# Optimization experiments

Measured on AMD Instinct MI355X. Metric: run time of the kernel, lower is better.

## Reference

```python
import jax, jax.numpy as jnp
import numpy as np
from jax import lax

DIM = 384
HEADS = 8
HEAD_DIM = DIM // HEADS
EPS = 1e-06


def setup_inputs() -> dict:
    key = jax.random.key(0)
    ks = jax.random.split(key, 16)
    B, N, C = 8, 4096, DIM
    s = 0.02
    inp = {
        "x": jax.random.normal(ks[0], (B, N, C), jnp.float32),
        "wq": jax.random.normal(ks[1], (C, C), jnp.float32) * s,
        "bq": jnp.zeros((C,), jnp.float32),
        "wk": jax.random.normal(ks[2], (C, C), jnp.float32) * s,
        "bk": jnp.zeros((C,), jnp.float32),
        "wv": jax.random.normal(ks[3], (C, C), jnp.float32) * s,
        "bv": jnp.zeros((C,), jnp.float32),
        "wg": jax.random.normal(ks[4], (C, C), jnp.float32) * s,
        "bg": jnp.zeros((C,), jnp.float32),
        "wo": jax.random.normal(ks[5], (C, C), jnp.float32) * s,
        "bo": jnp.zeros((C,), jnp.float32),
        "temperature": jnp.ones((HEADS, 1, 1), jnp.float32),
        "dw_w": jax.random.normal(ks[6], (C, 1, 3, 3), jnp.float32) * s,  # depthwise 3x3
        "dw_b": jnp.zeros((C,), jnp.float32),
        "pw_w": jax.random.normal(ks[7], (C, C), jnp.float32) * s,        # pointwise 1x1
        "pw_b": jnp.zeros((C,), jnp.float32),
    }
    return inp


def _phi(x):
    # exp(x - max) over last dim, numerically stable
    return jnp.exp(x - jnp.max(x, axis=-1, keepdims=True))


def _token_mixer(x, dw_w, dw_b, pw_w, pw_b):
    B, N, C = x.shape
    H = W = int(np.sqrt(N))
    feat = x.transpose(0, 2, 1).reshape(B, C, H, W)
    feat = lax.conv_general_dilated(
        feat, dw_w, window_strides=(1, 1), padding=((1, 1), (1, 1)),
        feature_group_count=C, dimension_numbers=("NCHW", "OIHW", "NCHW"))
    feat = feat + dw_b[None, :, None, None]
    feat = jnp.einsum("bchw,oc->bohw", feat, pw_w) + pw_b[None, :, None, None]
    return feat.reshape(B, C, N).transpose(0, 2, 1)


def reference(x, wq, bq, wk, bk, wv, bv, wg, bg, wo, bo, temperature,
              dw_w, dw_b, pw_w, pw_b):
    B, N, C = x.shape
    residual = x
    x = x + _token_mixer(x, dw_w, dw_b, pw_w, pw_b)

    def heads(y):  # [B,N,C] -> [B,H,N,d]
        return y.reshape(B, N, HEADS, HEAD_DIM).transpose(0, 2, 1, 3)

    q = heads(jnp.einsum("bnc,oc->bno", x, wq) + bq)
    k = heads(jnp.einsum("bnc,oc->bno", x, wk) + bk)
    v = heads(jnp.einsum("bnc,oc->bno", x, wv) + bv)
    g = heads(jnp.einsum("bnc,oc->bno", x, wg) + bg)

    q = _phi(q * temperature[None])       # temperature: [H,1,1] broadcasts over [B,H,N,d]
    k = _phi(k)
    v = v * jax.nn.sigmoid(g)

    kv = jnp.einsum("bhnd,bhne->bhde", k, v)     # [B,H,d,d]
    k_sum = jnp.sum(k, axis=2)                   # [B,H,d]
    num = jnp.einsum("bhnd,bhde->bhne", q, kv)   # [B,H,N,d]
    den = jnp.einsum("bhnd,bhd->bhn", q, k_sum)[..., None] + EPS
    out = num / den

    out = out.transpose(0, 2, 1, 3).reshape(B, N, C)
    out = jnp.einsum("bnc,oc->bno", out, wo) + bo
    return out + 0.0 * residual
```

## Files before the change

### kernel.cpp

```cpp
#include <hip/hip_runtime.h>
#include <math.h>

#define EPSF 1e-6f

typedef __attribute__((ext_vector_type(8))) short bf16x8;
typedef __attribute__((ext_vector_type(4))) float f32x4;
typedef unsigned short u16;
typedef unsigned int u32;

#define MFMA16(a,b,c) __builtin_amdgcn_mfma_f32_16x16x32_bf16((a),(b),(c),0,0,0)

__device__ __forceinline__ u16 f2bf(float f){
  u32 x = __builtin_bit_cast(u32, f);
  u32 r = (x + 0x7fffu + ((x >> 16) & 1u)) >> 16;
  return (u16)r;
}
__device__ __forceinline__ void gll16(const void* g, void* l){
  __builtin_amdgcn_global_load_lds(
      (const __attribute__((address_space(1))) u32*)g,
      (__attribute__((address_space(3))) u32*)l, 16, 0, 0);
}

__global__ __launch_bounds__(256) void k0_prep(
    const float* __restrict__ wq, const float* __restrict__ bq,
    const float* __restrict__ wk, const float* __restrict__ bk,
    const float* __restrict__ wv, const float* __restrict__ bv,
    const float* __restrict__ wg, const float* __restrict__ bg,
    const float* __restrict__ pw_w, const float* __restrict__ wo,
    u16* __restrict__ wpack, u16* __restrict__ pwb, u16* __restrict__ wob,
    float* __restrict__ bpack, float* __restrict__ kvacc, float* __restrict__ ksumacc)
{
  int idx = blockIdx.x*256 + threadIdx.x;
  const int NW = 1536*384;
  if (idx < NW) {
    int r = idx / 384, c = idx - r*384;
    int h = r / 192, s = (r % 192)/48, d = r % 48;
    const float* w = (s==0)?wq:(s==1)?wk:(s==2)?wv:wg;
    wpack[idx] = f2bf(w[(h*48+d)*384 + c]);
    if (c==0){
      const float* b = (s==0)?bq:(s==1)?bk:(s==2)?bv:bg;
      bpack[r] = b[h*48+d];
    }
  } else if (idx < NW + 147456) {
    pwb[idx - NW] = f2bf(pw_w[idx - NW]);
  } else if (idx < NW + 2*147456) {
    wob[idx - NW - 147456] = f2bf(wo[idx - NW - 147456]);
  } else if (idx < NW + 2*147456 + 147456) {
    kvacc[idx - NW - 2*147456] = 0.f;
  } else if (idx < NW + 2*147456 + 147456 + 3072) {
    ksumacc[idx - NW - 2*147456 - 147456] = 0.f;
  }
}

__global__ __launch_bounds__(256) void k1_dw(
    const float* __restrict__ x, const float* __restrict__ dw_w,
    const float* __restrict__ dw_b, u16* __restrict__ t)
{
  int idx = blockIdx.x*256 + threadIdx.x;
  int c4 = idx % 96; int rest = idx / 96;
  int jg = rest & 15; rest >>= 4;
  int i = rest & 63; int b = rest >> 6;
  int c0 = c4*4, j0 = jg*4;
  float wf[36];
  {
    const float4* wp = (const float4*)(dw_w + c0*9);
    #pragma unroll
    for (int k=0;k<9;k++){
      float4 v = wp[k];
      wf[4*k] = v.x; wf[4*k+1] = v.y; wf[4*k+2] = v.z; wf[4*k+3] = v.w;
    }
  }
  float4 bias = *(const float4*)(dw_b + c0);
  float acc[4][4];
  #pragma unroll
  for (int tk=0;tk<4;tk++){
    acc[tk][0]=bias.x; acc[tk][1]=bias.y; acc[tk][2]=bias.z; acc[tk][3]=bias.w;
  }
  const float* xb = x + ((size_t)b<<12)*384;
  #pragma unroll
  for (int di=-1; di<=1; ++di){
    int ii = i+di; if ((unsigned)ii >= 64u) continue;
    #pragma unroll
    for (int dj=-1; dj<=4; ++dj){
      int jj = j0+dj; if ((unsigned)jj >= 64u) continue;
      float4 xv = *(const float4*)(xb + (size_t)((ii<<6)+jj)*384 + c0);
      #pragma unroll
      for (int tk=0;tk<4;tk++){
        const int dd = dj - tk;
        if (dd < -1 || dd > 1) continue;
        const int tap = (di+1)*3 + (dd+1);
        acc[tk][0] = fmaf(xv.x, wf[0*9+tap], acc[tk][0]);
        acc[tk][1] = fmaf(xv.y, wf[1*9+tap], acc[tk][1]);
        acc[tk][2] = fmaf(xv.z, wf[2*9+tap], acc[tk][2]);
        acc[tk][3] = fmaf(xv.w, wf[3*9+tap], acc[tk][3]);
      }
    }
  }
  int mbase = (b<<12) + (i<<6) + j0;
  #pragma unroll
  for (int tk=0;tk<4;tk++){
    ushort4 o; o.x=f2bf(acc[tk][0]); o.y=f2bf(acc[tk][1]);
    o.z=f2bf(acc[tk][2]); o.w=f2bf(acc[tk][3]);
    *(ushort4*)(t + (size_t)(mbase+tk)*384 + c0) = o;
  }
}

__global__ __launch_bounds__(256) void k2_gemm_pw(
    const u16* __restrict__ t, const u16* __restrict__ pwb,
    const float* __restrict__ x, const float* __restrict__ pw_b,
    u16* __restrict__ xm)
{
  __shared__ __align__(16) u16 As[128*64];
  __shared__ __align__(16) u16 Bs[128*64];
  const int m0 = blockIdx.x * 128;
  const int n0 = blockIdx.y * 128;
  const int tid = threadIdx.x, w = tid>>6, l = tid&63;
  const int lc = l & 15, hi = l >> 4;
  const int osw = ((l&7) ^ (l>>3))*16;
  const f32x4 zf = {0.f,0.f,0.f,0.f};
  f32x4 acc[4][4];
  #pragma unroll
  for (int i=0;i<4;i++)
    #pragma unroll
    for (int j=0;j<4;j++) acc[i][j] = zf;

  for (int k0=0; k0<384; k0+=64) {
    #pragma unroll
    for (int i=0;i<4;i++){
      int ch = w*4+i;
      int row = ch*8 + (l>>3);
      gll16((const char*)t   + ((size_t)(m0+row)*384 + k0)*2 + osw, (char*)As + ch*1024);
      gll16((const char*)pwb + ((size_t)(n0+row)*384 + k0)*2 + osw, (char*)Bs + ch*1024);
    }
    __syncthreads();
    const int wr = (w>>1)*64, wc = (w&1)*64;
    #pragma unroll
    for (int kk=0; kk<64; kk+=32){
      const int sc = (((kk>>3)+hi) ^ (lc&7))*8;
      bf16x8 a[4], bb[4];
      #pragma unroll
      for (int i=0;i<4;i++) a[i]  = *(const bf16x8*)&As[(wr + i*16 + lc)*64 + sc];
      #pragma unroll
      for (int j=0;j<4;j++) bb[j] = *(const bf16x8*)&Bs[(wc + j*16 + lc)*64 + sc];
      #pragma unroll
      for (int i=0;i<4;i++)
        #pragma unroll
        for (int j=0;j<4;j++)
          acc[i][j] = MFMA16(a[i], bb[j], acc[i][j]);
    }
    __syncthreads();
  }
  const int wr=(w>>1)*64, wc=(w&1)*64;
  #pragma unroll
  for (int j=0;j<4;j++){
    int n = n0 + wc + j*16 + lc;
    float bias = pw_b[n];
    #pragma unroll
    for (int i=0;i<4;i++)
      #pragma unroll
      for (int r=0;r<4;r++){
        int m = m0 + wr + i*16 + hi*4 + r;
        float v = acc[i][j][r] + x[(size_t)m*384 + n] + bias;
        xm[(size_t)m*384 + n] = f2bf(v);
      }
  }
}

__global__ __launch_bounds__(256) void k3_gemm_qkvg(
    const u16* __restrict__ xm, const u16* __restrict__ wpack,
    const float* __restrict__ bpack, const float* __restrict__ temperature,
    u16* __restrict__ qh, float* __restrict__ kvacc, float* __restrict__ ksumacc)
{
  __shared__ __align__(16) u16 smem[40960];
  const int m0 = blockIdx.x * 128;
  const int h  = blockIdx.y;
  const int tid = threadIdx.x, w = tid>>6, l = tid&63;
  const int lc = l & 15, hi = l >> 4;
  const int osw = ((l&7) ^ (l>>3))*16;
  const f32x4 zf = {0.f,0.f,0.f,0.f};
  f32x4 acc[2][12];
  #pragma unroll
  for (int i=0;i<2;i++)
    #pragma unroll
    for (int j=0;j<12;j++) acc[i][j] = zf;

  const int arow = (w*4)*8 + (l>>3);
  const int brow = (w*6)*8 + (l>>3);

  #define K3_STAGE(T, BUF) do {                                                \
    const int k0_ = (T)*64;                                                    \
    char* Ab_ = (char*)(smem + (BUF)*8192);                                    \
    char* Bb_ = (char*)(smem + 16384 + (BUF)*12288);                           \
    _Pragma("unroll")                                                          \
    for (int i=0;i<4;i++)                                                      \
      gll16((const char*)xm + ((size_t)(m0+arow+i*8)*384 + k0_)*2 + osw,       \
            Ab_ + (w*4+i)*1024);                                               \
    _Pragma("unroll")                                                          \
    for (int i=0;i<6;i++)                                                      \
      gll16((const char*)wpack + ((size_t)(h*192+brow+i*8)*384 + k0_)*2 + osw, \
            Bb_ + (w*6+i)*1024);                                               \
  } while(0)

  K3_STAGE(0, 0);
  __syncthreads();
  int cur = 0;
  const int rbase = w*32;
  for (int t=0; t<6; ++t){
    if (t < 5) K3_STAGE(t+1, cur^1);
    const u16* Ab = smem + cur*8192;
    const u16* Bb = smem + 16384 + cur*12288;
    #pragma unroll
    for (int kk=0; kk<64; kk+=32){
      const int sc = (((kk>>3)+hi) ^ (lc&7))*8;
      bf16x8 a0 = *(const bf16x8*)&Ab[(rbase +      lc)*64 + sc];
      bf16x8 a1 = *(const bf16x8*)&Ab[(rbase + 16 + lc)*64 + sc];
      #pragma unroll
      for (int j=0;j<12;j++){
        bf16x8 bb = *(const bf16x8*)&Bb[(j*16 + lc)*64 + sc];
        acc[0][j] = MFMA16(a0, bb, acc[0][j]);
        acc[1][j] = MFMA16(a1, bb, acc[1][j]);
      }
    }
    __syncthreads();
    cur ^= 1;
  }
  #undef K3_STAGE

  const float tq = temperature[h];
  const int b = m0 >> 12;
  const size_t bh = (size_t)b*8 + h;
  const int bb0 = h*192;
  float biasq[3], biask[3], biasv[3], biasg[3];
  #pragma unroll
  for (int j=0;j<3;j++){
    biasq[j] = bpack[bb0       + j*16 + lc];
    biask[j] = bpack[bb0 + 48  + j*16 + lc];
    biasv[j] = bpack[bb0 + 96  + j*16 + lc];
    biasg[j] = bpack[bb0 + 144 + j*16 + lc];
  }
  u16* kT = smem;
  u16* vT = smem + 6528;
  float ksp[3] = {0.f, 0.f, 0.f};

  #pragma unroll
  for (int i=0;i<2;i++){
    ushort4 kst[3], vst[3];
    #pragma unroll
    for (int r=0;r<4;r++){
      int m = m0 + w*32 + i*16 + hi*4 + r;
      int n = m & 4095;
      size_t rowq = (bh*4096 + n)*64;
      float q0=(acc[i][0][r]+biasq[0])*tq;
      float q1=(acc[i][1][r]+biasq[1])*tq;
      float q2=(acc[i][2][r]+biasq[2])*tq;
      float mx = fmaxf(q0,fmaxf(q1,q2));
      mx = fmaxf(mx, __shfl_xor(mx,1,64));
      mx = fmaxf(mx, __shfl_xor(mx,2,64));
      mx = fmaxf(mx, __shfl_xor(mx,4,64));
      mx = fmaxf(mx, __shfl_xor(mx,8,64));
      qh[rowq +      lc] = f2bf(expf(q0-mx));
      qh[rowq + 16 + lc] = f2bf(expf(q1-mx));
      qh[rowq + 32 + lc] = f2bf(expf(q2-mx));
      qh[rowq + 48 + lc] = 0;
      float s0=acc[i][3][r]+biask[0];
      float s1=acc[i][4][r]+biask[1];
      float s2=acc[i][5][r]+biask[2];
      float mk = fmaxf(s0,fmaxf(s1,s2));
      mk = fmaxf(mk, __shfl_xor(mk,1,64));
      mk = fmaxf(mk, __shfl_xor(mk,2,64));
      mk = fmaxf(mk, __shfl_xor(mk,4,64));
      mk = fmaxf(mk, __shfl_xor(mk,8,64));
      float k0e = expf(s0-mk), k1e = expf(s1-mk), k2e = expf(s2-mk);
      ksp[0] += k0e; ksp[1] += k1e; ksp[2] += k2e;
      u16 kq0=f2bf(k0e), kq1=f2bf(k1e), kq2=f2bf(k2e);
      u16 vq[3];
      #pragma unroll
      for (int j=0;j<3;j++){
        float vv = acc[i][6+j][r] + biasv[j];
        float gg = acc[i][9+j][r] + biasg[j];
        float sg = 1.f/(1.f + expf(-gg));
        vq[j] = f2bf(vv*sg);
      }
      if (r==0){ kst[0].x=kq0; kst[1].x=kq1; kst[2].x=kq2; vst[0].x=vq[0]; vst[1].x=vq[1]; vst[2].x=vq[2]; }
      if (r==1){ kst[0].y=kq0; kst[1].y=kq1; kst[2].y=kq2; vst[0].y=vq[0]; vst[1].y=vq[1]; vst[2].y=vq[2]; }
      if (r==2){ kst[0].z=kq0; kst[1].z=kq1; kst[2].z=kq2; vst[0].z=vq[0]; vst[1].z=vq[1]; vst[2].z=vq[2]; }
      if (r==3){ kst[0].w=kq0; kst[1].w=kq1; kst[2].w=kq2; vst[0].w=vq[0]; vst[1].w=vq[1]; vst[2].w=vq[2]; }
    }
    int mb = w*32 + i*16 + hi*4;
    #pragma unroll
    for (int j=0;j<3;j++){
      *(ushort4*)&kT[(j*16+lc)*136 + mb] = kst[j];
      *(ushort4*)&vT[(j*16+lc)*136 + mb] = vst[j];
    }
  }
  __syncthreads();

  bf16x8 af[3], bfv[3];
  #pragma unroll
  for (int da=0;da<3;da++) af[da]  = *(const bf16x8*)&kT[(da*16+lc)*136 + w*32 + hi*8];
  #pragma unroll
  for (int eb=0;eb<3;eb++) bfv[eb] = *(const bf16x8*)&vT[(eb*16+lc)*136 + w*32 + hi*8];
  f32x4 a2[3][3];
  #pragma unroll
  for (int da=0;da<3;da++)
    #pragma unroll
    for (int eb=0;eb<3;eb++)
      a2[da][eb] = MFMA16(af[da], bfv[eb], zf);
  __syncthreads();
  float* pb = (float*)smem + w*2304;
  #pragma unroll
  for (int da=0;da<3;da++)
    #pragma unroll
    for (int eb=0;eb<3;eb++)
      #pragma unroll
      for (int rr=0;rr<4;rr++)
        pb[(da*16 + hi*4 + rr)*48 + eb*16 + lc] = a2[da][eb][rr];
  __syncthreads();
  float* p0 = (float*)smem;
  for (int u=tid; u<2304; u+=256){
    float s = p0[u] + p0[2304+u] + p0[4608+u] + p0[6912+u];
    atomicAdd(kvacc + bh*2304 + u, s);
  }
  #pragma unroll
  for (int j=0;j<3;j++){
    ksp[j] += __shfl_xor(ksp[j],16,64);
    ksp[j] += __shfl_xor(ksp[j],32,64);
  }
  if (hi==0){
    atomicAdd(ksumacc + bh*48 +      lc, ksp[0]);
    atomicAdd(ksumacc + bh*48 + 16 + lc, ksp[1]);
    atomicAdd(ksumacc + bh*48 + 32 + lc, ksp[2]);
  }
}

__global__ __launch_bounds__(256) void k5_red(
    const float* __restrict__ kvacc, const float* __restrict__ ksumacc,
    u16* __restrict__ kvp)
{
  int bh = blockIdx.x, tid = threadIdx.x;
  for (int u=tid; u<4096; u+=256){
    int e = u >> 6, d = u & 63;
    float v = 0.f;
    if (e < 48 && d < 48)       v = kvacc[(size_t)bh*2304 + d*48 + e];
    else if (e == 48 && d < 48) v = ksumacc[bh*48 + d];
    kvp[((size_t)bh*64 + e)*64 + d] = f2bf(v);
  }
}

__global__ __launch_bounds__(256) void k6_num(
    const u16* __restrict__ qh, const u16* __restrict__ kvp, u16* __restrict__ ah)
{
  __shared__ __align__(16) u16 As[256*64];
  __shared__ __align__(16) u16 Bs[64*64];
  const int bh = blockIdx.x >> 4, nc = blockIdx.x & 15;
  const int tid = threadIdx.x, w = tid>>6, l = tid&63;
  const int lc = l & 15, hi = l >> 4;
  const f32x4 zf = {0.f,0.f,0.f,0.f};
  const u16* gq = qh + ((size_t)bh*4096 + nc*256)*64;
  #pragma unroll
  for (int it=0; it<8; ++it){
    int s = it*256 + tid;
    int row = s>>3, c = s&7, g = c ^ (row&7);
    ((uint4*)As)[s] = *(const uint4*)(gq + (size_t)row*64 + g*8);
  }
  const u16* gk = kvp + (size_t)bh*4096;
  #pragma unroll
  for (int it=0; it<2; ++it){
    int s = it*256 + tid;
    int row = s>>3, c = s&7, g = c ^ (row&7);
    ((uint4*)Bs)[s] = *(const uint4*)(gk + (size_t)row*64 + g*8);
  }
  __syncthreads();
  f32x4 acc[4][4];
  #pragma unroll
  for (int i=0;i<4;i++)
    #pragma unroll
    for (int j=0;j<4;j++) acc[i][j] = zf;
  const int rbase = w*64;
  #pragma unroll
  for (int kk=0; kk<64; kk+=32){
    const int sc = (((kk>>3)+hi) ^ (lc&7))*8;
    bf16x8 a[4], bb[4];
    #pragma unroll
    for (int i=0;i<4;i++) a[i]  = *(const bf16x8*)&As[(rbase + i*16 + lc)*64 + sc];
    #pragma unroll
    for (int j=0;j<4;j++) bb[j] = *(const bf16x8*)&Bs[(j*16 + lc)*64 + sc];
    #pragma unroll
    for (int i=0;i<4;i++)
      #pragma unroll
      for (int j=0;j<4;j++)
        acc[i][j] = MFMA16(a[i], bb[j], acc[i][j]);
  }
  const int b = bh >> 3, h = bh & 7;
  #pragma unroll
  for (int i=0;i<4;i++){
    #pragma unroll
    for (int r=0;r<4;r++){
      float den = __shfl(acc[i][3][r], l & 48, 64) + EPSF;
      float rd = 1.f/den;
      int n = nc*256 + rbase + i*16 + hi*4 + r;
      size_t ob = ((size_t)b*4096 + n)*384 + h*48;
      ah[ob +      lc] = f2bf(acc[i][0][r]*rd);
      ah[ob + 16 + lc] = f2bf(acc[i][1][r]*rd);
      ah[ob + 32 + lc] = f2bf(acc[i][2][r]*rd);
    }
  }
}

__global__ __launch_bounds__(256) void k7_gemm_out(
    const u16* __restrict__ ah, const u16* __restrict__ wob,
    const float* __restrict__ bo, float* __restrict__ out)
{
  __shared__ __align__(16) u16 As[128*64];
  __shared__ __align__(16) u16 Bs[128*64];
  const int m0 = blockIdx.x * 128;
  const int n0 = blockIdx.y * 128;
  const int tid = threadIdx.x, w = tid>>6, l = tid&63;
  const int lc = l & 15, hi = l >> 4;
  const int osw = ((l&7) ^ (l>>3))*16;
  const f32x4 zf = {0.f,0.f,0.f,0.f};
  f32x4 acc[4][4];
  #pragma unroll
  for (int i=0;i<4;i++)
    #pragma unroll
    for (int j=0;j<4;j++) acc[i][j] = zf;

  for (int k0=0; k0<384; k0+=64) {
    #pragma unroll
    for (int i=0;i<4;i++){
      int ch = w*4+i;
      int row = ch*8 + (l>>3);
      gll16((const char*)ah  + ((size_t)(m0+row)*384 + k0)*2 + osw, (char*)As + ch*1024);
      gll16((const char*)wob + ((size_t)(n0+row)*384 + k0)*2 + osw, (char*)Bs + ch*1024);
    }
    __syncthreads();
    const int wr = (w>>1)*64, wc = (w&1)*64;
    #pragma unroll
    for (int kk=0; kk<64; kk+=32){
      const int sc = (((kk>>3)+hi) ^ (lc&7))*8;
      bf16x8 a[4], bb[4];
      #pragma unroll
      for (int i=0;i<4;i++) a[i]  = *(const bf16x8*)&As[(wr + i*16 + lc)*64 + sc];
      #pragma unroll
      for (int j=0;j<4;j++) bb[j] = *(const bf16x8*)&Bs[(wc + j*16 + lc)*64 + sc];
      #pragma unroll
      for (int i=0;i<4;i++)
        #pragma unroll
        for (int j=0;j<4;j++)
          acc[i][j] = MFMA16(a[i], bb[j], acc[i][j]);
    }
    __syncthreads();
  }
  const int wr=(w>>1)*64, wc=(w&1)*64;
  #pragma unroll
  for (int j=0;j<4;j++){
    int n = n0 + wc + j*16 + lc;
    float bias = bo[n];
    #pragma unroll
    for (int i=0;i<4;i++)
      #pragma unroll
      for (int r=0;r<4;r++){
        int m = m0 + wr + i*16 + hi*4 + r;
        out[(size_t)m*384 + n] = acc[i][j][r] + bias;
      }
  }
}

extern "C" void kernel_launch(void* const* d_in, const int* in_sizes, int n_in,
                              void* d_out, int out_size, void* d_ws, size_t ws_size,
                              hipStream_t stream)
{
  const float* x    = (const float*)d_in[0];
  const float* wq   = (const float*)d_in[1];
  const float* bq   = (const float*)d_in[2];
  const float* wk   = (const float*)d_in[3];
  const float* bk   = (const float*)d_in[4];
  const float* wv   = (const float*)d_in[5];
  const float* bv   = (const float*)d_in[6];
  const float* wg   = (const float*)d_in[7];
  const float* bg   = (const float*)d_in[8];
  const float* wo   = (const float*)d_in[9];
  const float* bo   = (const float*)d_in[10];
  const float* temp = (const float*)d_in[11];
  const float* dw_w = (const float*)d_in[12];
  const float* dw_b = (const float*)d_in[13];
  const float* pw_w = (const float*)d_in[14];
  const float* pw_b = (const float*)d_in[15];
  float* out = (float*)d_out;
  char* ws = (char*)d_ws;

  u16*   t       = (u16*)(ws + 0);
  u16*   xm      = (u16*)(ws + 25165824);
  u16*   qh      = (u16*)(ws + 50331648);
  u16*   wpack   = (u16*)(ws + 83886080);
  u16*   pwb     = (u16*)(ws + 85065728);
  u16*   wob     = (u16*)(ws + 85360640);
  float* bpack   = (float*)(ws + 85655552);
  float* kvacc   = (float*)(ws + 85661696);
  float* ksumacc = (float*)(ws + 86251520);
  u16*   kvp     = (u16*)(ws + 86263808);

  k0_prep<<<4044, 256, 0, stream>>>(wq,bq,wk,bk,wv,bv,wg,bg,pw_w,wo,
                                    wpack,pwb,wob,bpack,kvacc,ksumacc);
  k1_dw<<<3072, 256, 0, stream>>>(x, dw_w, dw_b, t);
  k2_gemm_pw<<<dim3(256,3), 256, 0, stream>>>(t, pwb, x, pw_b, xm);
  k3_gemm_qkvg<<<dim3(256,8), 256, 0, stream>>>(xm, wpack, bpack, temp, qh, kvacc, ksumacc);
  k5_red<<<64, 256, 0, stream>>>(kvacc, ksumacc, kvp);
  k6_num<<<1024, 256, 0, stream>>>(qh, kvp, t );
  k7_gemm_out<<<dim3(256,3), 256, 0, stream>>>(t, wob, bo, out);
}
```

Before: 190.9 us.

## Replace kv atomics with per-tile partial sums reduced in k5; drop q max-subtraction

k3 no longer atomically accumulates the kv and k-sum statistics into global buffers. Each block now writes its own partial tile into a scratch area that reuses the dead t region, and k5 sums the 32 partials per batch-head before packing. The zeroing of the accumulators in k0 is removed. This trades millions of contended global atomics for plain stores plus an extra 19MB read pass in k5. The per-row max subtraction for q is also dropped, since it cancels in num/den, which saves shuffles but risks exp overflow for large q.

New measurement: 186.6 us. 1.02x faster.

```diff
diff --git a/kernel.cpp b/kernel.cpp
--- a/kernel.cpp
+++ b/kernel.cpp
@@ -28,7 +28,7 @@
     const float* __restrict__ wg, const float* __restrict__ bg,
     const float* __restrict__ pw_w, const float* __restrict__ wo,
     u16* __restrict__ wpack, u16* __restrict__ pwb, u16* __restrict__ wob,
-    float* __restrict__ bpack, float* __restrict__ kvacc, float* __restrict__ ksumacc)
+    float* __restrict__ bpack)
 {
   int idx = blockIdx.x*256 + threadIdx.x;
   const int NW = 1536*384;
@@ -45,10 +45,6 @@
     pwb[idx - NW] = f2bf(pw_w[idx - NW]);
   } else if (idx < NW + 2*147456) {
     wob[idx - NW - 147456] = f2bf(wo[idx - NW - 147456]);
-  } else if (idx < NW + 2*147456 + 147456) {
-    kvacc[idx - NW - 2*147456] = 0.f;
-  } else if (idx < NW + 2*147456 + 147456 + 3072) {
-    ksumacc[idx - NW - 2*147456 - 147456] = 0.f;
   }
 }
 
@@ -169,7 +165,7 @@
 __global__ __launch_bounds__(256) void k3_gemm_qkvg(
     const u16* __restrict__ xm, const u16* __restrict__ wpack,
     const float* __restrict__ bpack, const float* __restrict__ temperature,
-    u16* __restrict__ qh, float* __restrict__ kvacc, float* __restrict__ ksumacc)
+    u16* __restrict__ qh, float* __restrict__ pkv, float* __restrict__ pks)
 {
   __shared__ __align__(16) u16 smem[40960];
   const int m0 = blockIdx.x * 128;
@@ -228,6 +224,7 @@
 
   const float tq = temperature[h];
   const int b = m0 >> 12;
+  const int mtile = (m0 >> 7) & 31;
   const size_t bh = (size_t)b*8 + h;
   const int bb0 = h*192;
   float biasq[3], biask[3], biasv[3], biasg[3];
@@ -253,14 +250,9 @@
       float q0=(acc[i][0][r]+biasq[0])*tq;
       float q1=(acc[i][1][r]+biasq[1])*tq;
       float q2=(acc[i][2][r]+biasq[2])*tq;
-      float mx = fmaxf(q0,fmaxf(q1,q2));
-      mx = fmaxf(mx, __shfl_xor(mx,1,64));
-      mx = fmaxf(mx, __shfl_xor(mx,2,64));
-      mx = fmaxf(mx, __shfl_xor(mx,4,64));
-      mx = fmaxf(mx, __shfl_xor(mx,8,64));
-      qh[rowq +      lc] = f2bf(expf(q0-mx));
-      qh[rowq + 16 + lc] = f2bf(expf(q1-mx));
-      qh[rowq + 32 + lc] = f2bf(expf(q2-mx));
+      qh[rowq +      lc] = f2bf(expf(q0));
+      qh[rowq + 16 + lc] = f2bf(expf(q1));
+      qh[rowq + 32 + lc] = f2bf(expf(q2));
       qh[rowq + 48 + lc] = 0;
       float s0=acc[i][3][r]+biask[0];
       float s1=acc[i][4][r]+biask[1];
@@ -316,33 +308,60 @@
       for (int rr=0;rr<4;rr++)
         pb[(da*16 + hi*4 + rr)*48 + eb*16 + lc] = a2[da][eb][rr];
   __syncthreads();
-  float* p0 = (float*)smem;
-  for (int u=tid; u<2304; u+=256){
-    float s = p0[u] + p0[2304+u] + p0[4608+u] + p0[6912+u];
-    atomicAdd(kvacc + bh*2304 + u, s);
+  {
+    float* p0 = (float*)smem;
+    float* dst = pkv + ((size_t)bh*32 + mtile)*2304;
+    for (int u=tid; u<2304; u+=256)
+      dst[u] = p0[u] + p0[2304+u] + p0[4608+u] + p0[6912+u];
   }
   #pragma unroll
   for (int j=0;j<3;j++){
     ksp[j] += __shfl_xor(ksp[j],16,64);
     ksp[j] += __shfl_xor(ksp[j],32,64);
   }
-  if (hi==0){
-    atomicAdd(ksumacc + bh*48 +      lc, ksp[0]);
-    atomicAdd(ksumacc + bh*48 + 16 + lc, ksp[1]);
-    atomicAdd(ksumacc + bh*48 + 32 + lc, ksp[2]);
+  if (hi==0 && w==0){
+    float* ds = pks + ((size_t)bh*32 + mtile)*48;
+    ds[lc] = ksp[0]; ds[16+lc] = ksp[1]; ds[32+lc] = ksp[2];
+  }
+  __syncthreads();
+  {
+    float* kr = (float*)smem;
+    if (hi==0){ kr[w*48+lc]=ksp[0]; kr[w*48+16+lc]=ksp[1]; kr[w*48+32+lc]=ksp[2]; }
+    __syncthreads();
+    if (tid < 48){
+      float* ds = pks + ((size_t)bh*32 + mtile)*48;
+      ds[tid] = kr[tid] + kr[48+tid] + kr[96+tid] + kr[144+tid];
+    }
   }
 }
 
 __global__ __launch_bounds__(256) void k5_red(
-    const float* __restrict__ kvacc, const float* __restrict__ ksumacc,
+    const float* __restrict__ pkv, const float* __restrict__ pks,
     u16* __restrict__ kvp)
 {
+  __shared__ float sm[2304];
+  __shared__ float ks[48];
   int bh = blockIdx.x, tid = threadIdx.x;
+  const float* base = pkv + (size_t)bh*32*2304;
+  for (int u=tid; u<2304; u+=256){
+    float v = 0.f;
+    #pragma unroll
+    for (int m=0;m<32;m++) v += base[(size_t)m*2304 + u];
+    sm[u] = v;
+  }
+  if (tid < 48){
+    const float* bk = pks + (size_t)bh*32*48 + tid;
+    float v = 0.f;
+    #pragma unroll
+    for (int m=0;m<32;m++) v += bk[m*48];
+    ks[tid] = v;
+  }
+  __syncthreads();
   for (int u=tid; u<4096; u+=256){
     int e = u >> 6, d = u & 63;
     float v = 0.f;
-    if (e < 48 && d < 48)       v = kvacc[(size_t)bh*2304 + d*48 + e];
-    else if (e == 48 && d < 48) v = ksumacc[bh*48 + d];
+    if (e < 48 && d < 48)       v = sm[d*48 + e];
+    else if (e == 48 && d < 48) v = ks[d];
     kvp[((size_t)bh*64 + e)*64 + d] = f2bf(v);
   }
 }
@@ -490,22 +509,23 @@
   char* ws = (char*)d_ws;
 
   u16*   t       = (u16*)(ws + 0);
+  float* pkv     = (float*)(ws + 0);
+  float* pks     = (float*)(ws + 18874368);
+  u16*   ah      = (u16*)(ws + 0);
   u16*   xm      = (u16*)(ws + 25165824);
   u16*   qh      = (u16*)(ws + 50331648);
   u16*   wpack   = (u16*)(ws + 83886080);
   u16*   pwb     = (u16*)(ws + 85065728);
   u16*   wob     = (u16*)(ws + 85360640);
   float* bpack   = (float*)(ws + 85655552);
-  float* kvacc   = (float*)(ws + 85661696);
-  float* ksumacc = (float*)(ws + 86251520);
-  u16*   kvp     = (u16*)(ws + 86263808);
-
-  k0_prep<<<4044, 256, 0, stream>>>(wq,bq,wk,bk,wv,bv,wg,bg,pw_w,wo,
-                                    wpack,pwb,wob,bpack,kvacc,ksumacc);
+  u16*   kvp     = (u16*)(ws + 85661696);
+
+  k0_prep<<<3456, 256, 0, stream>>>(wq,bq,wk,bk,wv,bv,wg,bg,pw_w,wo,
+                                    wpack,pwb,wob,bpack);
   k1_dw<<<3072, 256, 0, stream>>>(x, dw_w, dw_b, t);
   k2_gemm_pw<<<dim3(256,3), 256, 0, stream>>>(t, pwb, x, pw_b, xm);
-  k3_gemm_qkvg<<<dim3(256,8), 256, 0, stream>>>(xm, wpack, bpack, temp, qh, kvacc, ksumacc);
-  k5_red<<<64, 256, 0, stream>>>(kvacc, ksumacc, kvp);
-  k6_num<<<1024, 256, 0, stream>>>(qh, kvp, t );
-  k7_gemm_out<<<dim3(256,3), 256, 0, stream>>>(t, wob, bo, out);
-}
+  k3_gemm_qkvg<<<dim3(256,8), 256, 0, stream>>>(xm, wpack, bpack, temp, qh, pkv, pks);
+  k5_red<<<64, 256, 0, stream>>>(pkv, pks, kvp);
+  k6_num<<<1024, 256, 0, stream>>>(qh, kvp, ah);
+  k7_gemm_out<<<dim3(256,3), 256, 0, stream>>>(ah, wob, bo, out);
+}
```
